# Optimization experiments

Hardware: AMD Instinct MI355X
Metric: run time of the kernel (lower is better)

## Reference

```python
import jax, jax.numpy as jnp
import numpy as np

DEPTH = 256
HEADS = 8
K = 128          # kernel_size == attended axis length (height)
DH = DEPTH // HEADS  # 32
EPS = 1e-5


def _bn(x, gamma, beta, axes):
    # training-mode batch norm (biased variance), per-channel on axis 1
    mean = jnp.mean(x, axis=axes, keepdims=True)
    var = jnp.var(x, axis=axes, keepdims=True)
    shape = [1] * x.ndim
    shape[1] = x.shape[1]
    g = gamma.reshape(shape)
    b = beta.reshape(shape)
    return (x - mean) * jax.lax.rsqrt(var + EPS) * g + b


def setup_inputs() -> dict:
    key = jax.random.key(0)
    ks = jax.random.split(key, 3)
    x = jax.random.normal(ks[0], (2, DEPTH, K, K), dtype=jnp.float32)
    w_kqv = jax.random.normal(ks[1], (2 * DEPTH, DEPTH), dtype=jnp.float32) * 0.05
    rel_encoding = jax.random.normal(ks[2], (2 * DH, 2 * K - 1), dtype=jnp.float32)
    return {
        "x": x,
        "w_kqv": w_kqv,
        "kqv_gamma": jnp.ones((2 * DEPTH,), jnp.float32),
        "kqv_beta": jnp.zeros((2 * DEPTH,), jnp.float32),
        "logits_gamma": jnp.ones((3 * HEADS,), jnp.float32),
        "logits_beta": jnp.zeros((3 * HEADS,), jnp.float32),
        "rel_encoding": rel_encoding,
    }


def reference(x, w_kqv, kqv_gamma, kqv_beta, logits_gamma, logits_beta, rel_encoding):
    B, C, H, W = x.shape  # height_dim=True path
    # (B,C,H,W) -> (B,W,C,H) -> (B*W, C, H)
    xf = jnp.transpose(x, (0, 3, 1, 2)).reshape(B * W, C, H)
    # 1x1 conv == channel matmul
    kqv = jnp.einsum('oc,bch->boh', w_kqv, xf)  # (BW, 2*depth, H)
    kqv = _bn(kqv, kqv_gamma, kqv_beta, axes=(0, 2))
    kqv = kqv.reshape(B * W, HEADS, 2 * DH, H)
    k = kqv[:, :, : DH // 2]            # (BW, h, dh/2, H)
    q = kqv[:, :, DH // 2: DH]          # (BW, h, dh/2, H)
    v = kqv[:, :, DH:]                  # (BW, h, dh,   H)

    # relative position gather: (2*dh, 2K-1) -> (2*dh, K, K)
    idx = (jnp.arange(K)[None, :] - jnp.arange(K)[:, None] + K - 1).reshape(-1)
    rel = rel_encoding[:, idx].reshape(2 * DH, K, K)
    q_enc = rel[: DH // 2]
    k_enc = rel[DH // 2: DH]
    v_enc = rel[DH:]

    qk = jnp.einsum('bhdx,bhdy->bhxy', q, k)
    qr = jnp.einsum('bhdx,dxy->bhxy', q, q_enc)
    kr = jnp.swapaxes(jnp.einsum('bhdx,dxy->bhxy', k, k_enc), 2, 3)
    logits = jnp.concatenate([qk, qr, kr], axis=1)  # (BW, 3*h, K, K)
    logits = _bn(logits, logits_gamma, logits_beta, axes=(0, 2, 3))
    logits = logits.reshape(B * W, 3, HEADS, H, H).sum(axis=1)
    weights = jax.nn.softmax(logits, axis=3)  # (BW, h, K, K)

    attn = jnp.einsum('bhxy,bhdy->bhdx', weights, v)         # (BW, h, dh, H)
    attn_enc = jnp.einsum('bhxy,dxy->bhdx', weights, v_enc)  # (BW, h, dh, H)
    out = (attn + attn_enc).reshape(B, W, DEPTH, H)  # cat+reshape+sum(dim=-2) == add
    out = jnp.transpose(out, (0, 2, 3, 1))  # (B, depth, H, W)
    return out
```

## Files before the change

### kernel.cpp

```cpp
#include <hip/hip_runtime.h>
#include <hip/hip_bf16.h>

#define H 128
#define NB 256
#define OC 512
#define CIN 256
#define NN 16384
#define EPS 1e-5f

#define EQG_OFF 524288
#define EKG_OFF 589824
#define EVG_OFF 655360

typedef __attribute__((ext_vector_type(4))) float f32x4;
typedef __attribute__((ext_vector_type(8))) short bf16x8;
typedef unsigned short u16x8 __attribute__((ext_vector_type(8)));

__device__ __forceinline__ float bf2f(unsigned short u){
    return __uint_as_float(((unsigned int)u) << 16);
}
__device__ __forceinline__ unsigned short f2bf(float f){
    unsigned int r;
    asm("v_cvt_pk_bf16_f32 %0, %1, %2" : "=v"(r) : "v"(f), "v"(f));
    return (unsigned short)r;
}
__device__ __forceinline__ float ldin(const void* p, size_t i, bool f32){
    return f32 ? ((const float*)p)[i] : bf2f(((const unsigned short*)p)[i]);
}
__device__ __forceinline__ short ld_bf16(const void* p, size_t i, bool f32){
    if (f32) return (short)f2bf(((const float*)p)[i]);
    return ((const short*)p)[i];
}
__device__ __forceinline__ bool probe_f32(const void* gamma_ones){
    return *(const unsigned int*)gamma_ones == 0x3F800000u;
}

template<bool F32>
__device__ __forceinline__ void gemm_body(const void* __restrict__ w,
                                          const void* __restrict__ x,
                                          unsigned short* __restrict__ c1,
                                          short (*As)[128][40], short (*Bs)[128][40])
{
    const int m0 = blockIdx.x * 128;
    const int n0 = blockIdx.y * 128;
    const int b0 = blockIdx.z;
    const int t  = threadIdx.x;
    const int lane = t & 63, wv = t >> 6;
    const int wm = wv & 1, wn = wv >> 1;
    const int lm = lane & 15, quad = lane >> 4;
    const size_t xb = (size_t)b0 * CIN * NN;
    const int am = t >> 1, ak = (t & 1) * 16;
    const int bn = t & 127, bk = (t >> 7) * 16;

    float4 pa[4]; float pb[16];
    u16x8 qa[2]; unsigned short qb[16];

    auto load_tile = [&](int k0){
        if constexpr (F32){
            const float* wp = (const float*)w + (size_t)(m0+am)*CIN + k0 + ak;
            #pragma unroll
            for (int q=0;q<4;q++) pa[q] = *(const float4*)(wp + 4*q);
            const float* xp = (const float*)x + xb + (size_t)(k0+bk)*NN + n0 + bn;
            #pragma unroll
            for (int i=0;i<16;i++) pb[i] = xp[(size_t)i*NN];
        } else {
            const unsigned short* wp = (const unsigned short*)w + (size_t)(m0+am)*CIN + k0 + ak;
            qa[0] = *(const u16x8*)wp; qa[1] = *(const u16x8*)(wp+8);
            const unsigned short* xp = (const unsigned short*)x + xb + (size_t)(k0+bk)*NN + n0 + bn;
            #pragma unroll
            for (int i=0;i<16;i++) qb[i] = xp[(size_t)i*NN];
        }
    };
    auto store_tile = [&](int buf){
        if constexpr (F32){
            short ta[16];
            #pragma unroll
            for (int q=0;q<4;q++){
                ta[4*q+0]=(short)f2bf(pa[q].x); ta[4*q+1]=(short)f2bf(pa[q].y);
                ta[4*q+2]=(short)f2bf(pa[q].z); ta[4*q+3]=(short)f2bf(pa[q].w);
            }
            *(bf16x8*)&As[buf][am][ak]   = *(bf16x8*)&ta[0];
            *(bf16x8*)&As[buf][am][ak+8] = *(bf16x8*)&ta[8];
            short tb[16];
            #pragma unroll
            for (int i=0;i<16;i++) tb[i] = (short)f2bf(pb[i]);
            *(bf16x8*)&Bs[buf][bn][bk]   = *(bf16x8*)&tb[0];
            *(bf16x8*)&Bs[buf][bn][bk+8] = *(bf16x8*)&tb[8];
        } else {
            *(u16x8*)&As[buf][am][ak]   = qa[0];
            *(u16x8*)&As[buf][am][ak+8] = qa[1];
            *(u16x8*)&Bs[buf][bn][bk]   = *(u16x8*)&qb[0];
            *(u16x8*)&Bs[buf][bn][bk+8] = *(u16x8*)&qb[8];
        }
    };

    f32x4 acc[4][4];
    #pragma unroll
    for (int i=0;i<4;i++)
        #pragma unroll
        for (int j=0;j<4;j++) acc[i][j]=(f32x4){0,0,0,0};

    load_tile(0); store_tile(0); __syncthreads();
    for (int kk=0; kk<8; ++kk){
        const int cur = kk & 1;
        if (kk < 7) load_tile((kk+1)*32);
        bf16x8 af[4], bfB[4];
        #pragma unroll
        for (int i=0;i<4;i++) af[i]  = *(const bf16x8*)&As[cur][wm*64 + i*16 + lm][quad*8];
        #pragma unroll
        for (int j=0;j<4;j++) bfB[j] = *(const bf16x8*)&Bs[cur][wn*64 + j*16 + lm][quad*8];
        #pragma unroll
        for (int i=0;i<4;i++)
            #pragma unroll
            for (int j=0;j<4;j++)
                acc[i][j] = __builtin_amdgcn_mfma_f32_16x16x32_bf16(af[i], bfB[j], acc[i][j], 0,0,0);
        if (kk < 7) store_tile(cur ^ 1);
        __syncthreads();
    }
    #pragma unroll
    for (int i=0;i<4;i++){
        #pragma unroll
        for (int j=0;j<4;j++){
            int n = n0 + wn*64 + j*16 + lm;
            #pragma unroll
            for (int r=0;r<4;r++){
                int m = m0 + wm*64 + i*16 + quad*4 + r;
                c1[((size_t)b0*OC + m)*NN + n] = f2bf(acc[i][j][r]);
            }
        }
    }
}

__global__ __launch_bounds__(256) void k_gemm(const void* __restrict__ w,
                                              const void* __restrict__ x,
                                              unsigned short* __restrict__ c1,
                                              const void* __restrict__ probe)
{
    __shared__ short As[2][128][40];
    __shared__ short Bs[2][128][40];
    if (probe_f32(probe)) gemm_body<true >(w, x, c1, As, Bs);
    else                  gemm_body<false>(w, x, c1, As, Bs);
}

__global__ __launch_bounds__(256) void k_bn_transpose(const unsigned short* __restrict__ c1,
        unsigned short* __restrict__ kqvt,
        const void* __restrict__ gamma, const void* __restrict__ beta)
{
    __shared__ short T[128][130];
    __shared__ float red[8];
    __shared__ float sc_sh[2];
    const bool f32 = probe_f32(gamma);
    const int o  = blockIdx.x;
    const int b0 = blockIdx.y;
    const int t = threadIdx.x;
    const int lane = t & 63, wv = t >> 6;
    const u16x8* r08 = (const u16x8*)(c1 + (size_t)o*NN);
    const u16x8* r18 = (const u16x8*)(c1 + ((size_t)OC + o)*NN);
    float sp[4] = {0,0,0,0}, qp[4] = {0,0,0,0};
    #pragma unroll
    for (int i=0;i<8;i++){
        u16x8 a = r08[t + i*256];
        u16x8 b = r18[t + i*256];
        #pragma unroll
        for (int e=0;e<8;e++){
            float va = bf2f(a[e]); sp[e&3] += va; qp[e&3] = fmaf(va,va,qp[e&3]);
            float vb = bf2f(b[e]); sp[e&3] += vb; qp[e&3] = fmaf(vb,vb,qp[e&3]);
        }
    }
    float s = (sp[0]+sp[1])+(sp[2]+sp[3]);
    float ss = (qp[0]+qp[1])+(qp[2]+qp[3]);
    #pragma unroll
    for (int off=1; off<64; off<<=1){ s += __shfl_xor(s,off); ss += __shfl_xor(ss,off); }
    if (lane==0){ red[wv*2] = s; red[wv*2+1] = ss; }
    __syncthreads();
    if (t==0){
        float st=0.f, sq=0.f;
        for (int i=0;i<4;i++){ st += red[i*2]; sq += red[i*2+1]; }
        float mean = st * (1.f/32768.f);
        float var  = sq * (1.f/32768.f) - mean*mean;
        float scale = ldin(gamma, o, f32) * rsqrtf(var + EPS);
        sc_sh[0] = scale;
        sc_sh[1] = ldin(beta, o, f32) - mean*scale;
    }
    __syncthreads();
    const float scale = sc_sh[0], shift = sc_sh[1];
    const u16x8* r8 = b0 ? r18 : r08;
    #pragma unroll
    for (int i=0;i<8;i++){
        int vi = t + i*256;
        u16x8 a = r8[vi];
        int n0_ = vi*8;
        int h = n0_ >> 7, ww = n0_ & 127;
        #pragma unroll
        for (int e=0;e<8;e++) T[ww+e][h] = (short)a[e];
    }
    __syncthreads();
    #pragma unroll
    for (int i=0;i<8;i++){
        int vi = t + i*256;
        int ww = vi >> 4, h8 = (vi & 15)*8;
        u16x8 tv = *(const u16x8*)&T[ww][h8];
        unsigned short outv[8];
        #pragma unroll
        for (int e=0;e<8;e++)
            outv[e] = f2bf(fmaf(bf2f((unsigned short)tv[e]), scale, shift));
        *(u16x8*)&kqvt[(((size_t)(b0*128 + ww))*OC + o)*H + h8] = *(u16x8*)outv;
    }
}

__global__ __launch_bounds__(256) void k_encpre(const void* __restrict__ relenc,
        float* __restrict__ ws, const void* __restrict__ probe)
{
    __shared__ float E[16][256];
    const bool f32 = probe_f32(probe);
    const int grp = blockIdx.x;
    const int t = threadIdx.x;
    if (grp == 2){
        unsigned short* ev = (unsigned short*)ws + EVG_OFF;
        for (int i = t; i < 32*264; i += 256){
            int d = i / 264, j = i - d*264;
            ev[i] = (j < 255) ? (unsigned short)ld_bf16(relenc, (size_t)(32+d)*255 + j, f32) : 0;
        }
        return;
    }
    for (int i = t; i < 16*255; i += 256){
        int d = i / 255, j = i - d*255;
        E[d][j] = bf2f((unsigned short)ld_bf16(relenc, (size_t)(grp*16 + d)*255 + j, f32));
    }
    __syncthreads();
    float* Rout = ws + 256  + grp*2048;
    float* Cout = ws + 8192 + grp*32768;
    {
        const int d = t >> 4, e = t & 15;
        const float* Ed = E[d]; const float* Ee = E[e];
        float c = 0.f;
        for (int j = 0; j < 128; ++j) c = fmaf(Ed[j], Ee[j], c);
        float* Cp = Cout + (d*16+e)*128;
        Cp[127] = c;
        for (int xx = 126; xx >= 0; --xx){
            c += Ed[254-xx]*Ee[254-xx] - Ed[126-xx]*Ee[126-xx];
            Cp[xx] = c;
        }
    }
    if (t < 16){
        const float* Ed = E[t];
        float r = 0.f;
        for (int j = 0; j < 128; ++j) r += Ed[j];
        float* Rp = Rout + t*128;
        Rp[127] = r;
        for (int xx = 126; xx >= 0; --xx){
            r += Ed[254-xx] - Ed[126-xx];
            Rp[xx] = r;
        }
    }
}

__global__ __launch_bounds__(256) void k_stats2(const unsigned short* __restrict__ kqvt,
        const float* __restrict__ ws, float* __restrict__ stats)
{
    __shared__ short QK[2][16][128];
    __shared__ float wr[4][6];
    const int b = blockIdx.x >> 3, head = blockIdx.x & 7;
    const int t = threadIdx.x;
    const int lane = t & 63, wv = t >> 6;
    const int lm = lane & 15, quad = lane >> 4;
    const unsigned short* base = kqvt + ((size_t)b*OC + head*64)*H;
    for (int i = t; i < 512; i += 256){
        int arr = i >> 8, d = (i >> 4) & 15, c = i & 15;
        *(u16x8*)&QK[arr][d][c*8] = *(const u16x8*)&base[(size_t)(arr*16 + d)*H + c*8];
    }
    __syncthreads();

    float s_qk = 0.f, q_qk = 0.f;
    if (wv == 0){
        f32x4 gq  = (f32x4){0,0,0,0}, gk  = (f32x4){0,0,0,0};
        f32x4 gq1 = (f32x4){0,0,0,0}, gk1 = (f32x4){0,0,0,0};
        bf16x8 ones;
        #pragma unroll
        for (int i=0;i<8;i++) ones[i] = (short)0x3F80;
        #pragma unroll
        for (int xt=0; xt<4; ++xt){
            bf16x8 fq = *(const bf16x8*)&QK[1][lm][xt*32 + quad*8];
            bf16x8 fk = *(const bf16x8*)&QK[0][lm][xt*32 + quad*8];
            gq  = __builtin_amdgcn_mfma_f32_16x16x32_bf16(fq, fq,   gq,  0,0,0);
            gk  = __builtin_amdgcn_mfma_f32_16x16x32_bf16(fk, fk,   gk,  0,0,0);
            gq1 = __builtin_amdgcn_mfma_f32_16x16x32_bf16(fq, ones, gq1, 0,0,0);
            gk1 = __builtin_amdgcn_mfma_f32_16x16x32_bf16(fk, ones, gk1, 0,0,0);
        }
        #pragma unroll
        for (int r=0;r<4;r++) q_qk += gq[r]*gk[r];
        if (lm == 0){
            #pragma unroll
            for (int r=0;r<4;r++) s_qk += gq1[r]*gk1[r];
        }
    }

    const int half = t >> 7;
    const int x = t & 127;
    float col[16];
    #pragma unroll
    for (int d=0; d<16; ++d) col[d] = bf2f((unsigned short)QK[1-half][d][x]);
    const float* Rp = ws + 256  + half*2048;
    const float* Cp = ws + 8192 + half*32768;
    float sr = 0.f;
    #pragma unroll
    for (int d=0; d<16; ++d) sr = fmaf(col[d], Rp[d*128 + x], sr);
    float q2p[4] = {0,0,0,0};
    for (int d=0; d<16; ++d){
        float qd = col[d];
        #pragma unroll
        for (int e=0; e<16; ++e)
            q2p[e&3] = fmaf(qd*col[e], Cp[(d*16+e)*128 + x], q2p[e&3]);
    }
    float q2 = (q2p[0]+q2p[1]) + (q2p[2]+q2p[3]);
    float s_qr = half ? 0.f : sr,  q_qr = half ? 0.f : q2;
    float s_kr = half ? sr : 0.f,  q_kr = half ? q2 : 0.f;

    #pragma unroll
    for (int off=1; off<64; off<<=1){
        s_qk += __shfl_xor(s_qk,off); q_qk += __shfl_xor(q_qk,off);
        s_qr += __shfl_xor(s_qr,off); q_qr += __shfl_xor(q_qr,off);
        s_kr += __shfl_xor(s_kr,off); q_kr += __shfl_xor(q_kr,off);
    }
    if (lane==0){ wr[wv][0]=s_qk; wr[wv][1]=s_qr; wr[wv][2]=s_kr;
                  wr[wv][3]=q_qk; wr[wv][4]=q_qr; wr[wv][5]=q_kr; }
    __syncthreads();
    if (t==0){
        float a0=0,a1=0,a2=0,b0_=0,b1=0,b2=0;
        for (int i=0;i<4;i++){ a0+=wr[i][0]; a1+=wr[i][1]; a2+=wr[i][2];
                               b0_+=wr[i][3]; b1+=wr[i][4]; b2+=wr[i][5]; }
        atomicAdd(&stats[head],      a0);
        atomicAdd(&stats[8+head],    a1);
        atomicAdd(&stats[16+head],   a2);
        atomicAdd(&stats[24+head],   b0_);
        atomicAdd(&stats[32+head],   b1);
        atomicAdd(&stats[40+head],   b2);
    }
}

__global__ void k_scales(const float* __restrict__ stats, float* __restrict__ scales,
                         const void* __restrict__ gamma_l, const void* __restrict__ probe)
{
    const bool f32 = probe_f32(probe);
    int t = threadIdx.x;
    if (t < 24){
        const float inv_cnt = 1.f/4194304.f;
        float mean = stats[t]*inv_cnt;
        float var  = stats[24+t]*inv_cnt - mean*mean;
        scales[t] = ldin(gamma_l, t, f32) * rsqrtf(var + EPS);
    }
}

__global__ void k_escale(const void* __restrict__ relenc, const float* __restrict__ scales,
                         unsigned short* __restrict__ etab, const void* __restrict__ probe)
{
    const bool f32 = probe_f32(probe);
    const int head = blockIdx.x;
    const int t = threadIdx.x;
    const float s1 = scales[8+head], s2 = scales[16+head];
    unsigned short* eq = etab + EQG_OFF + head*8192;
    unsigned short* ek = etab + EKG_OFF + head*8192;
    for (int i = t; i < 8192; i += 256){
        int j = i >> 5, c = i & 31;
        unsigned short vq = 0, vk = 0;
        if (c < 16 && j < 255){
            vq = f2bf(s1 * ldin(relenc, (size_t)c*255 + j, f32));
            vk = f2bf(s2 * ldin(relenc, (size_t)(16+c)*255 + j, f32));
        }
        eq[i] = vq; ek[i] = vk;
    }
}

__global__ __launch_bounds__(256) void k_attn(const unsigned short* __restrict__ kqvt,
        const unsigned short* __restrict__ etab,
        const float* __restrict__ scales,
        void* __restrict__ outp,
        const void* __restrict__ probe)
{
    __shared__ short KA[128][24];
    __shared__ short RW[128][130];
    __shared__ alignas(16) short ZED[16];
    const bool f32 = probe_f32(probe);
    const int blk = blockIdx.x;
    const int b = blk >> 3, head = blk & 7;
    const int b0 = b >> 7, w = b & 127;
    const int t = threadIdx.x;
    const int lane = t & 63, wv = t >> 6;
    const int lm = lane & 15, quad = lane >> 4;
    const unsigned short* base = kqvt + ((size_t)b*OC + head*64)*H;
    const float s0 = scales[head];
    const unsigned short* EQg = etab + EQG_OFF + (size_t)head*8192;
    const unsigned short* EKg = etab + EKG_OFF + (size_t)head*8192;
    const unsigned short* EVg = etab + EVG_OFF;

    {
        int dd = t & 15, xg = (t >> 4) * 8;
        u16x8 kv = *(const u16x8*)&base[dd*H + xg];
        #pragma unroll
        for (int e=0;e<8;e++) KA[xg+e][dd] = (short)kv[e];
    }
    bf16x8 aq[2];
    #pragma unroll
    for (int u=0;u<2;u++){
        aq[u] = (bf16x8){0,0,0,0,0,0,0,0};
        if (quad < 2){
            const int x = (2*wv+u)*16 + lm;
            const unsigned short* qp = base + (16+quad*8)*H + x;
            #pragma unroll
            for (int e=0;e<8;e++) aq[u][e] = (short)qp[(size_t)e*H];
        }
    }
    if (t < 16) ZED[t] = 0;
    __syncthreads();

    bf16x8 akk[2];
    #pragma unroll
    for (int u=0;u<2;u++){
        akk[u] = (bf16x8){0,0,0,0,0,0,0,0};
        if (quad < 2) akk[u] = *(const bf16x8*)&KA[(2*wv+u)*16 + lm][quad*8];
    }

    f32x4 qacc[2][8];
    #pragma unroll
    for (int u=0;u<2;u++){
        const int mt = 2*wv + u;
        #pragma unroll
        for (int yt=0; yt<8; ++yt){
            const short* pb = (quad < 2) ? &KA[yt*16 + lm][quad*8] : &ZED[0];
            bf16x8 bk = *(const bf16x8*)pb;
            qacc[u][yt] = __builtin_amdgcn_mfma_f32_16x16x32_bf16(aq[u], bk,
                            (f32x4){0.f,0.f,0.f,0.f}, 0,0,0);
        }
        #pragma unroll
        for (int jj=0; jj<9; ++jj){
            const int jt = 7 - mt + jj;
            bf16x8 bq = *(const bf16x8*)&EQg[(size_t)(jt*16 + lm)*32 + quad*8];
            f32x4 cq = __builtin_amdgcn_mfma_f32_16x16x32_bf16(aq[u], bq,
                         (f32x4){0.f,0.f,0.f,0.f}, 0,0,0);
            int j = jt*16 + lm;
            #pragma unroll
            for (int r=0;r<4;r++){
                int x = mt*16 + quad*4 + r;
                int y = x + j - 127;
                if ((unsigned)y < 128u) RW[x][y] = (short)f2bf(cq[r]);
            }
        }
    }
    __syncthreads();

    #pragma unroll
    for (int u=0;u<2;u++){
        const int mt = 2*wv + u;
        #pragma unroll
        for (int jj=0; jj<9; ++jj){
            const int jt = 7 - mt + jj;
            bf16x8 bkE = *(const bf16x8*)&EKg[(size_t)(jt*16 + lm)*32 + quad*8];
            f32x4 ck = __builtin_amdgcn_mfma_f32_16x16x32_bf16(akk[u], bkE,
                         (f32x4){0.f,0.f,0.f,0.f}, 0,0,0);
            int j = jt*16 + lm;
            #pragma unroll
            for (int r=0;r<4;r++){
                int y = mt*16 + quad*4 + r;
                int x = y + j - 127;
                if ((unsigned)x < 128u){
                    float cur = bf2f((unsigned short)RW[x][y]);
                    RW[x][y] = (short)f2bf(cur + ck[r]);
                }
            }
        }
    }
    __syncthreads();

    #pragma unroll
    for (int u=0;u<2;u++){
        const int mt = 2*wv + u;
        #pragma unroll
        for (int r=0;r<4;r++){
            const int x = mt*16 + quad*4 + r;
            float v[8]; float mx = -1e30f;
            #pragma unroll
            for (int yt=0; yt<8; ++yt){
                v[yt] = fmaf(s0, qacc[u][yt][r], bf2f((unsigned short)RW[x][yt*16 + lm]));
                mx = fmaxf(mx, v[yt]);
            }
            mx = fmaxf(mx, __shfl_xor(mx,1));
            mx = fmaxf(mx, __shfl_xor(mx,2));
            mx = fmaxf(mx, __shfl_xor(mx,4));
            mx = fmaxf(mx, __shfl_xor(mx,8));
            float sum = 0.f;
            #pragma unroll
            for (int yt=0; yt<8; ++yt){ v[yt] = __expf(v[yt]-mx); sum += v[yt]; }
            sum += __shfl_xor(sum,1);
            sum += __shfl_xor(sum,2);
            sum += __shfl_xor(sum,4);
            sum += __shfl_xor(sum,8);
            float inv = 1.f/sum;
            #pragma unroll
            for (int yt=0; yt<8; ++yt)
                RW[x][yt*16 + lm] = (short)f2bf(v[yt]*inv);
        }
    }
    __syncthreads();

    f32x4 o[2][2];
    #pragma unroll
    for (int u=0;u<2;u++){ o[u][0]=(f32x4){0,0,0,0}; o[u][1]=(f32x4){0,0,0,0}; }
    #pragma unroll
    for (int kt=0; kt<4; ++kt){
        bf16x8 bv0 = *(const bf16x8*)&base[(size_t)(32+lm)*H + kt*32 + quad*8];
        bf16x8 bv1 = *(const bf16x8*)&base[(size_t)(48+lm)*H + kt*32 + quad*8];
        #pragma unroll
        for (int u=0;u<2;u++){
            bf16x8 aw = *(const bf16x8*)&RW[(2*wv+u)*16 + lm][kt*32 + quad*8];
            o[u][0] = __builtin_amdgcn_mfma_f32_16x16x32_bf16(aw, bv0, o[u][0], 0,0,0);
            o[u][1] = __builtin_amdgcn_mfma_f32_16x16x32_bf16(aw, bv1, o[u][1], 0,0,0);
        }
    }
    #pragma unroll
    for (int u=0;u<2;u++){
        const int mt = 2*wv + u;
        const int ktlo = (112 - mt*16) >> 5;
        const int xg = mt*16 + lm;
        #pragma unroll
        for (int jj=0; jj<5; ++jj){
            const int kt = ktlo + jj;
            bf16x8 be0 = *(const bf16x8*)&EVg[(size_t)lm*264      + kt*32 + quad*8];
            bf16x8 be1 = *(const bf16x8*)&EVg[(size_t)(16+lm)*264 + kt*32 + quad*8];
            int y0 = xg + kt*32 + quad*8 - 127;
            short g[8];
            #pragma unroll
            for (int jjj=0;jjj<8;jjj++){
                int y = y0 + jjj;
                g[jjj] = ((unsigned)y < 128u) ? RW[xg][y] : (short)0;
            }
            bf16x8 ag = *(bf16x8*)g;
            o[u][0] = __builtin_amdgcn_mfma_f32_16x16x32_bf16(ag, be0, o[u][0], 0,0,0);
            o[u][1] = __builtin_amdgcn_mfma_f32_16x16x32_bf16(ag, be1, o[u][1], 0,0,0);
        }
    }
    #pragma unroll
    for (int u=0;u<2;u++){
        #pragma unroll
        for (int nt=0; nt<2; ++nt){
            int d = nt*16 + lm;
            size_t cb = ((size_t)(b0*256 + head*32 + d))*16384 + (size_t)w;
            #pragma unroll
            for (int r=0;r<4;r++){
                int x = (2*wv+u)*16 + quad*4 + r;
                if (f32) ((float*)outp)[cb + (size_t)x*128] = o[u][nt][r];
                else ((unsigned short*)outp)[cb + (size_t)x*128] = f2bf(o[u][nt][r]);
            }
        }
    }
}

extern "C" void kernel_launch(void* const* d_in, const int* in_sizes, int n_in,
                              void* d_out, int out_size, void* d_ws, size_t ws_size,
                              hipStream_t stream)
{
    (void)in_sizes; (void)n_in; (void)out_size;
    const void* x      = d_in[0];
    const void* w_kqv  = d_in[1];
    const void* kqv_g  = d_in[2];
    const void* kqv_b  = d_in[3];
    const void* log_g  = d_in[4];
    const void* relenc = d_in[6];

    if (ws_size < (size_t)64*1024*1024) return;
    unsigned short* C1   = (unsigned short*)d_ws;
    unsigned short* KQVT = C1 + 16777216;
    float* WS     = (float*)d_ws;
    float* STATS  = WS;
    float* SCALES = WS + 48;
    unsigned short* ETAB = (unsigned short*)d_ws;

    dim3 g1(OC/128, NN/128, 2);
    k_gemm<<<g1, 256, 0, stream>>>(w_kqv, x, C1, kqv_g);
    k_bn_transpose<<<dim3(512,2), 256, 0, stream>>>(C1, KQVT, kqv_g, kqv_b);
    hipMemsetAsync(STATS, 0, 48*sizeof(float), stream);
    k_encpre<<<3, 256, 0, stream>>>(relenc, WS, kqv_g);
    k_stats2<<<2048, 256, 0, stream>>>(KQVT, WS, STATS);
    k_scales<<<1, 64, 0, stream>>>(STATS, SCALES, log_g, kqv_g);
    k_escale<<<8, 256, 0, stream>>>(relenc, SCALES, ETAB, kqv_g);
    k_attn<<<2048, 256, 0, stream>>>(KQVT, ETAB, SCALES, d_out, kqv_g);
}
```

Measured before the change: 345.0 us.

## Swizzle GEMM block mapping per XCD, pack bf16 conversions, exploit symmetric quadratic form

The GEMM grid is flattened to 1D and remapped so each XCD (assigned round-robin by block id) works on a contiguous range of n tiles with all m tiles. This aims to improve L2 reuse of the activation tiles. The fp32→bf16 conversion packs two values per cvt instruction. The stats kernel's 16x16 quadratic form now uses its symmetry, roughly halving the FMAs and loads, which assumes the coefficient table is symmetric.

Result: no change. 346.8 us (+0.5%).

```diff
diff --git a/kernel.cpp b/kernel.cpp
--- a/kernel.cpp
+++ b/kernel.cpp
@@ -15,6 +15,7 @@
 typedef __attribute__((ext_vector_type(4))) float f32x4;
 typedef __attribute__((ext_vector_type(8))) short bf16x8;
 typedef unsigned short u16x8 __attribute__((ext_vector_type(8)));
+typedef unsigned int u32x4 __attribute__((ext_vector_type(4)));
 
 __device__ __forceinline__ float bf2f(unsigned short u){
     return __uint_as_float(((unsigned int)u) << 16);
@@ -24,6 +25,11 @@
     asm("v_cvt_pk_bf16_f32 %0, %1, %2" : "=v"(r) : "v"(f), "v"(f));
     return (unsigned short)r;
 }
+__device__ __forceinline__ unsigned int f2bf2(float a, float b){
+    unsigned int r;
+    asm("v_cvt_pk_bf16_f32 %0, %1, %2" : "=v"(r) : "v"(a), "v"(b));
+    return r;
+}
 __device__ __forceinline__ float ldin(const void* p, size_t i, bool f32){
     return f32 ? ((const float*)p)[i] : bf2f(((const unsigned short*)p)[i]);
 }
@@ -39,11 +45,9 @@
 __device__ __forceinline__ void gemm_body(const void* __restrict__ w,
                                           const void* __restrict__ x,
                                           unsigned short* __restrict__ c1,
-                                          short (*As)[128][40], short (*Bs)[128][40])
-{
-    const int m0 = blockIdx.x * 128;
-    const int n0 = blockIdx.y * 128;
-    const int b0 = blockIdx.z;
+                                          short (*As)[128][40], short (*Bs)[128][40],
+                                          int m0, int n0, int b0)
+{
     const int t  = threadIdx.x;
     const int lane = t & 63, wv = t >> 6;
     const int wm = wv & 1, wn = wv >> 1;
@@ -73,19 +77,20 @@
     };
     auto store_tile = [&](int buf){
         if constexpr (F32){
-            short ta[16];
-            #pragma unroll
-            for (int q=0;q<4;q++){
-                ta[4*q+0]=(short)f2bf(pa[q].x); ta[4*q+1]=(short)f2bf(pa[q].y);
-                ta[4*q+2]=(short)f2bf(pa[q].z); ta[4*q+3]=(short)f2bf(pa[q].w);
-            }
-            *(bf16x8*)&As[buf][am][ak]   = *(bf16x8*)&ta[0];
-            *(bf16x8*)&As[buf][am][ak+8] = *(bf16x8*)&ta[8];
-            short tb[16];
-            #pragma unroll
-            for (int i=0;i<16;i++) tb[i] = (short)f2bf(pb[i]);
-            *(bf16x8*)&Bs[buf][bn][bk]   = *(bf16x8*)&tb[0];
-            *(bf16x8*)&Bs[buf][bn][bk+8] = *(bf16x8*)&tb[8];
+            u32x4 ua0, ua1;
+            ua0[0]=f2bf2(pa[0].x,pa[0].y); ua0[1]=f2bf2(pa[0].z,pa[0].w);
+            ua0[2]=f2bf2(pa[1].x,pa[1].y); ua0[3]=f2bf2(pa[1].z,pa[1].w);
+            ua1[0]=f2bf2(pa[2].x,pa[2].y); ua1[1]=f2bf2(pa[2].z,pa[2].w);
+            ua1[2]=f2bf2(pa[3].x,pa[3].y); ua1[3]=f2bf2(pa[3].z,pa[3].w);
+            *(u32x4*)&As[buf][am][ak]   = ua0;
+            *(u32x4*)&As[buf][am][ak+8] = ua1;
+            u32x4 ub0, ub1;
+            #pragma unroll
+            for (int i=0;i<4;i++) ub0[i] = f2bf2(pb[2*i], pb[2*i+1]);
+            #pragma unroll
+            for (int i=0;i<4;i++) ub1[i] = f2bf2(pb[8+2*i], pb[8+2*i+1]);
+            *(u32x4*)&Bs[buf][bn][bk]   = ub0;
+            *(u32x4*)&Bs[buf][bn][bk+8] = ub1;
         } else {
             *(u16x8*)&As[buf][am][ak]   = qa[0];
             *(u16x8*)&As[buf][am][ak+8] = qa[1];
@@ -138,8 +143,13 @@
 {
     __shared__ short As[2][128][40];
     __shared__ short Bs[2][128][40];
-    if (probe_f32(probe)) gemm_body<true >(w, x, c1, As, Bs);
-    else                  gemm_body<false>(w, x, c1, As, Bs);
+    const int bid = blockIdx.x;
+    const int swz = (bid & 7)*128 + (bid >> 3);
+    const int m0 = (swz & 3)*128;
+    const int n0 = ((swz >> 2) & 127)*128;
+    const int b0 = swz >> 9;
+    if (probe_f32(probe)) gemm_body<true >(w, x, c1, As, Bs, m0, n0, b0);
+    else                  gemm_body<false>(w, x, c1, As, Bs, m0, n0, b0);
 }
 
 __global__ __launch_bounds__(256) void k_bn_transpose(const unsigned short* __restrict__ c1,
@@ -306,11 +316,13 @@
     #pragma unroll
     for (int d=0; d<16; ++d) sr = fmaf(col[d], Rp[d*128 + x], sr);
     float q2p[4] = {0,0,0,0};
+    #pragma unroll
     for (int d=0; d<16; ++d){
         float qd = col[d];
-        #pragma unroll
-        for (int e=0; e<16; ++e)
-            q2p[e&3] = fmaf(qd*col[e], Cp[(d*16+e)*128 + x], q2p[e&3]);
+        q2p[d&3] = fmaf(qd*qd, Cp[(d*17)*128 + x], q2p[d&3]);
+        #pragma unroll
+        for (int e=d+1; e<16; ++e)
+            q2p[e&3] = fmaf(2.f*qd*col[e], Cp[(d*16+e)*128 + x], q2p[e&3]);
     }
     float q2 = (q2p[0]+q2p[1]) + (q2p[2]+q2p[3]);
     float s_qr = half ? 0.f : sr,  q_qr = half ? 0.f : q2;
@@ -574,8 +586,7 @@
     float* SCALES = WS + 48;
     unsigned short* ETAB = (unsigned short*)d_ws;
 
-    dim3 g1(OC/128, NN/128, 2);
-    k_gemm<<<g1, 256, 0, stream>>>(w_kqv, x, C1, kqv_g);
+    k_gemm<<<1024, 256, 0, stream>>>(w_kqv, x, C1, kqv_g);
     k_bn_transpose<<<dim3(512,2), 256, 0, stream>>>(C1, KQVT, kqv_g, kqv_b);
     hipMemsetAsync(STATS, 0, 48*sizeof(float), stream);
     k_encpre<<<3, 256, 0, stream>>>(relenc, WS, kqv_g);
```
